# Kernel tuning notes

Measured on AMD Instinct MI355X. Metric: run time of the kernel, lower is better.

The kernel has to match this reference:

```python
import jax, jax.numpy as jnp
import numpy as np

S, B, D = 2048, 1, 4096
H, HKV, DH = 32, 8, 128
THETA = 10000.0


def _rope_tables(seq_len, dim, theta):
    inv_freq = 1.0 / (theta ** (jnp.arange(0, dim, 2, dtype=jnp.float32) / dim))
    freqs = jnp.arange(seq_len, dtype=jnp.float32)[:, None] * inv_freq[None, :]  # [S, DH/2]
    return jnp.cos(freqs), jnp.sin(freqs)


def _apply_rope(x, cos, sin):
    # x: [B, H, S, DH]; non-interleaved (flash_attn interleaved=False) rotation
    half = x.shape[-1] // 2
    x1, x2 = x[..., :half], x[..., half:]
    c = cos[None, None, :, :]
    s = sin[None, None, :, :]
    return jnp.concatenate([x1 * c - x2 * s, x2 * c + x1 * s], axis=-1)


def setup_inputs() -> dict:
    key = jax.random.key(0)
    k1, k2, k3 = jax.random.split(key, 3)
    hidden_states = jax.random.normal(k1, (S, B, D), dtype=jnp.float32)
    W_qkv = jax.random.normal(k2, (D, (H + 2 * HKV) * DH), dtype=jnp.float32) * 0.02
    W_o = jax.random.normal(k3, (H * DH, D), dtype=jnp.float32) * 0.02
    sequence_mask = jnp.ones((B, S), dtype=jnp.int32)
    return {"hidden_states": hidden_states, "sequence_mask": sequence_mask,
            "W_qkv": W_qkv, "W_o": W_o}


def reference(hidden_states, sequence_mask, W_qkv, W_o):
    s, b, _ = hidden_states.shape
    qkv = hidden_states @ W_qkv  # [S, B, (H+2*HKV)*DH]
    q, k, v = jnp.split(qkv, [H * DH, H * DH + HKV * DH], axis=-1)
    q = q.reshape(s, b, H, DH).transpose(1, 2, 0, 3)    # [B, H, S, DH]
    k = k.reshape(s, b, HKV, DH).transpose(1, 2, 0, 3)  # [B, HKV, S, DH]
    v = v.reshape(s, b, HKV, DH).transpose(1, 2, 0, 3)

    cos, sin = _rope_tables(s, DH, THETA)
    q = _apply_rope(q, cos, sin)
    k = _apply_rope(k, cos, sin)

    # GQA: repeat kv heads
    rep = H // HKV
    k = jnp.repeat(k, rep, axis=1)  # [B, H, S, DH]
    v = jnp.repeat(v, rep, axis=1)

    scale = 1.0 / jnp.sqrt(jnp.asarray(DH, dtype=q.dtype))
    scores = jnp.einsum('bhqd,bhkd->bhqk', q, k) * scale
    causal = jnp.tril(jnp.ones((s, s), dtype=bool))
    scores = jnp.where(causal[None, None, :, :], scores, jnp.finfo(scores.dtype).min)
    attn = jax.nn.softmax(scores, axis=-1)
    ctx = jnp.einsum('bhqk,bhkd->bhqd', attn, v)  # [B, H, S, DH]
    ctx = ctx.transpose(2, 0, 1, 3).reshape(s, b, H * DH)  # [S, B, H*DH]
    out = ctx @ W_o  # [S, B, D]
    return out
```

## Files before the change

### kernel.cpp

```cpp
#include <hip/hip_runtime.h>

typedef unsigned short u16;
typedef __bf16 bf16x8 __attribute__((ext_vector_type(8)));
typedef float f32x4 __attribute__((ext_vector_type(4)));
typedef u16 u16x4 __attribute__((ext_vector_type(4)));

constexpr int SEQ = 2048;
constexpr int NQKV = 6144;

__device__ __forceinline__ float bf2f(u16 x) {
    unsigned int u = ((unsigned int)x) << 16;
    return __builtin_bit_cast(float, u);
}
__device__ __forceinline__ u16 f2bf(float f) {
    unsigned int u = __builtin_bit_cast(unsigned int, f);
    u += 0x7FFF + ((u >> 16) & 1);
    return (u16)(u >> 16);
}

__device__ __forceinline__ void gload16(const void* g, void* l) {
    void* gg = const_cast<void*>(g);
    __builtin_amdgcn_global_load_lds(
        (__attribute__((address_space(1))) void*)gg,
        (__attribute__((address_space(3))) void*)l, 16, 0, 0);
}

__device__ __forceinline__ void gatebar(int G) {
    if (G == 8) asm volatile("s_waitcnt vmcnt(8)" ::: "memory");
    else if (G == 4) asm volatile("s_waitcnt vmcnt(4)" ::: "memory");
    else if (G == 3) asm volatile("s_waitcnt vmcnt(3)" ::: "memory");
    else if (G == 2) asm volatile("s_waitcnt vmcnt(2)" ::: "memory");
    else asm volatile("s_waitcnt vmcnt(0)" ::: "memory");
    __builtin_amdgcn_sched_barrier(0);
    __builtin_amdgcn_s_barrier();
    __builtin_amdgcn_sched_barrier(0);
}

__global__ void rope_table_k(float* __restrict__ tab) {
    int idx = blockIdx.x * 256 + threadIdx.x;
    if (idx >= SEQ * 64) return;
    int s = idx >> 6;
    int i = idx & 63;
    float invf = expf(-(float)i * (float)(1.0 / 64.0) * logf(10000.0f));
    float ang = (float)s * invf;
    float sv, cv;
    sincosf(ang, &sv, &cv);
    tab[idx * 2] = cv;
    tab[idx * 2 + 1] = sv;
}

__global__ __launch_bounds__(256) void cast_k(const float* __restrict__ src,
                                              u16* __restrict__ dst, int n4) {
    int i = blockIdx.x * 256 + threadIdx.x;
    if (i >= n4) return;
    f32x4 v = *(const f32x4*)&src[(size_t)i * 4];
    u16x4 o;
#pragma unroll
    for (int j = 0; j < 4; ++j) o[j] = f2bf(v[j]);
    *(u16x4*)&dst[(size_t)i * 4] = o;
}

__global__ __launch_bounds__(256) void transpose_cast_k(const float* __restrict__ src,
                                                        u16* __restrict__ dst, int R, int C) {
    __shared__ u16 tile[64][65];
    int t = threadIdx.x;
    int bx = blockIdx.x, by = blockIdx.y;
    int r0 = by * 64, c0 = bx * 64;
#pragma unroll
    for (int it = 0; it < 4; ++it) {
        int row = it * 16 + (t >> 4);
        int col = (t & 15) * 4;
        f32x4 v = *(const f32x4*)&src[(size_t)(r0 + row) * C + c0 + col];
        tile[row][col] = f2bf(v[0]); tile[row][col + 1] = f2bf(v[1]);
        tile[row][col + 2] = f2bf(v[2]); tile[row][col + 3] = f2bf(v[3]);
    }
    __syncthreads();
#pragma unroll
    for (int it = 0; it < 4; ++it) {
        int orow = it * 16 + (t >> 4);
        int ocol = (t & 15) * 4;
        u16x4 v;
        v[0] = tile[ocol][orow]; v[1] = tile[ocol + 1][orow];
        v[2] = tile[ocol + 2][orow]; v[3] = tile[ocol + 3][orow];
        *(u16x4*)&dst[(size_t)(c0 + orow) * R + r0 + ocol] = v;
    }
}

__global__ __launch_bounds__(256) void transpose_vt_k(const u16* __restrict__ QKV,
                                                      u16* __restrict__ VTg) {
    __shared__ u16 tile[64][65];
    int t = threadIdx.x;
    int s0 = blockIdx.x * 64;
    int hv = blockIdx.y >> 1;
    int d0 = (blockIdx.y & 1) * 64;
    const u16* src = QKV + (size_t)s0 * NQKV + 5120 + hv * 128 + d0;
#pragma unroll
    for (int it = 0; it < 4; ++it) {
        int row = it * 16 + (t >> 4);
        int col = (t & 15) * 4;
        u16x4 v = *(const u16x4*)&src[(size_t)row * NQKV + col];
        tile[row][col] = v[0]; tile[row][col + 1] = v[1];
        tile[row][col + 2] = v[2]; tile[row][col + 3] = v[3];
    }
    __syncthreads();
    u16* dst = VTg + (size_t)hv * 128 * SEQ + (size_t)d0 * SEQ + s0;
#pragma unroll
    for (int it = 0; it < 4; ++it) {
        int orow = it * 16 + (t >> 4);
        int ocol = (t & 15) * 4;
        u16x4 v;
        v[0] = tile[ocol][orow]; v[1] = tile[ocol + 1][orow];
        v[2] = tile[ocol + 2][orow]; v[3] = tile[ocol + 3][orow];
        *(u16x4*)&dst[(size_t)orow * SEQ + ocol] = v;
    }
}

__global__ __launch_bounds__(512, 2) void gemm1_big_k(const u16* __restrict__ A,
                                                      const u16* __restrict__ BT,
                                                      u16* __restrict__ C) {
    constexpr int K = 4096, N = 6144;
    constexpr int SBUF = 57344;
    __shared__ alignas(16) char lds[2 * SBUF];

    int t = threadIdx.x;
    int lane = t & 63, w = t >> 6;
    int wr = w >> 2, wc = w & 3;
    int l15 = lane & 15, l4 = lane >> 4;

    int wg = blockIdx.x;
    int xcd = wg & 7, j = wg >> 3;
    int bm = ((xcd >> 2) << 2) + (j >> 3);
    int bn = ((xcd & 3) << 3) + (j & 7);

    const u16* Ab = A + (size_t)bm * 256 * K;
    const u16* Bb = BT + (size_t)bn * 192 * K;

    const u16* ga[4]; int da[4];
#pragma unroll
    for (int i = 0; i < 4; ++i) {
        int c = t + i * 512;
        int row = c >> 3;
        int ch = (c & 7) ^ (row & 7);
        ga[i] = Ab + (size_t)row * K + ch * 8;
        da[i] = c * 16;
    }
    const u16* gb[3]; int db[3];
#pragma unroll
    for (int i = 0; i < 3; ++i) {
        int c = t + i * 512;
        int row = c >> 3;
        int ch = (c & 7) ^ (row & 7);
        gb[i] = Bb + (size_t)row * K + ch * 8;
        db[i] = 32768 + c * 16;
    }

    auto stage = [&](int kt) {
        char* L = lds + (kt & 1) * SBUF;
        int ko = kt * 64;
#pragma unroll
        for (int i = 0; i < 4; ++i) gload16(ga[i] + ko, L + da[i]);
#pragma unroll
        for (int i = 0; i < 3; ++i) gload16(gb[i] + ko, L + db[i]);
    };

    f32x4 acc[8][3];
#pragma unroll
    for (int i = 0; i < 8; ++i)
#pragma unroll
        for (int j2 = 0; j2 < 3; ++j2) acc[i][j2] = f32x4{0.f, 0.f, 0.f, 0.f};

    int arow[8];
#pragma unroll
    for (int fm = 0; fm < 8; ++fm) arow[fm] = wr * 128 + fm * 16 + l15;
    int brow[3];
#pragma unroll
    for (int fn = 0; fn < 3; ++fn) brow[fn] = wc * 48 + fn * 16 + l15;

    stage(0);
    gatebar(0);

    for (int kt = 0; kt < 64; ++kt) {
        const u16* L = (const u16*)(lds + (kt & 1) * SBUF);
        if (kt + 1 < 64) stage(kt + 1);
        bf16x8 bf[3][2];
#pragma unroll
        for (int fn = 0; fn < 3; ++fn)
#pragma unroll
            for (int kk = 0; kk < 2; ++kk) {
                int ch = (kk * 4 + l4) ^ (brow[fn] & 7);
                bf[fn][kk] = *(const bf16x8*)&L[16384 + brow[fn] * 64 + ch * 8];
            }
#pragma unroll
        for (int p = 0; p < 4; ++p) {
            bf16x8 af[2][2];
#pragma unroll
            for (int f2 = 0; f2 < 2; ++f2)
#pragma unroll
                for (int kk = 0; kk < 2; ++kk) {
                    int r = arow[p * 2 + f2];
                    int ch = (kk * 4 + l4) ^ (r & 7);
                    af[f2][kk] = *(const bf16x8*)&L[r * 64 + ch * 8];
                }
            __builtin_amdgcn_s_setprio(1);
#pragma unroll
            for (int f2 = 0; f2 < 2; ++f2)
#pragma unroll
                for (int kk = 0; kk < 2; ++kk)
#pragma unroll
                    for (int fn = 0; fn < 3; ++fn)
                        acc[p * 2 + f2][fn] = __builtin_amdgcn_mfma_f32_16x16x32_bf16(
                            af[f2][kk], bf[fn][kk], acc[p * 2 + f2][fn], 0, 0, 0);
            __builtin_amdgcn_s_setprio(0);
        }
        gatebar(0);
    }

#pragma unroll
    for (int fm = 0; fm < 8; ++fm)
#pragma unroll
        for (int fn = 0; fn < 3; ++fn)
#pragma unroll
            for (int i = 0; i < 4; ++i) {
                int row = bm * 256 + wr * 128 + fm * 16 + l4 * 4 + i;
                int col = bn * 192 + wc * 48 + fn * 16 + l15;
                C[(size_t)row * N + col] = f2bf(acc[fm][fn][i]);
            }
}

__global__ __launch_bounds__(512, 2) void gemm2_big_k(const u16* __restrict__ A,
                                                      const u16* __restrict__ BT,
                                                      float* __restrict__ C) {
    constexpr int K = 4096, N = 4096;
    constexpr int SBUF = 49152;
    __shared__ alignas(16) char lds[2 * SBUF];

    int t = threadIdx.x;
    int lane = t & 63, w = t >> 6;
    int wr = w >> 2, wc = w & 3;
    int l15 = lane & 15, l4 = lane >> 4;

    int wg = blockIdx.x;
    int xcd = wg & 7, j = wg >> 3;
    int bm = ((xcd >> 2) << 2) + (j >> 3);
    int bn = ((xcd & 3) << 3) + (j & 7);

    const u16* Ab = A + (size_t)bm * 256 * K;
    const u16* Bb = BT + (size_t)bn * 128 * K;

    const u16* ga[4]; int da[4];
#pragma unroll
    for (int i = 0; i < 4; ++i) {
        int c = t + i * 512;
        int row = c >> 3;
        int ch = (c & 7) ^ (row & 7);
        ga[i] = Ab + (size_t)row * K + ch * 8;
        da[i] = c * 16;
    }
    const u16* gb[2]; int db[2];
#pragma unroll
    for (int i = 0; i < 2; ++i) {
        int c = t + i * 512;
        int row = c >> 3;
        int ch = (c & 7) ^ (row & 7);
        gb[i] = Bb + (size_t)row * K + ch * 8;
        db[i] = 32768 + c * 16;
    }

    auto stage = [&](int kt) {
        char* L = lds + (kt & 1) * SBUF;
        int ko = kt * 64;
#pragma unroll
        for (int i = 0; i < 4; ++i) gload16(ga[i] + ko, L + da[i]);
#pragma unroll
        for (int i = 0; i < 2; ++i) gload16(gb[i] + ko, L + db[i]);
    };

    f32x4 acc[8][2];
#pragma unroll
    for (int i = 0; i < 8; ++i)
#pragma unroll
        for (int j2 = 0; j2 < 2; ++j2) acc[i][j2] = f32x4{0.f, 0.f, 0.f, 0.f};

    int arow[8];
#pragma unroll
    for (int fm = 0; fm < 8; ++fm) arow[fm] = wr * 128 + fm * 16 + l15;
    int brow[2];
#pragma unroll
    for (int fn = 0; fn < 2; ++fn) brow[fn] = wc * 32 + fn * 16 + l15;

    stage(0);
    gatebar(0);

    for (int kt = 0; kt < 64; ++kt) {
        const u16* L = (const u16*)(lds + (kt & 1) * SBUF);
        if (kt + 1 < 64) stage(kt + 1);
        bf16x8 bf[2][2];
#pragma unroll
        for (int fn = 0; fn < 2; ++fn)
#pragma unroll
            for (int kk = 0; kk < 2; ++kk) {
                int ch = (kk * 4 + l4) ^ (brow[fn] & 7);
                bf[fn][kk] = *(const bf16x8*)&L[16384 + brow[fn] * 64 + ch * 8];
            }
#pragma unroll
        for (int p = 0; p < 4; ++p) {
            bf16x8 af[2][2];
#pragma unroll
            for (int f2 = 0; f2 < 2; ++f2)
#pragma unroll
                for (int kk = 0; kk < 2; ++kk) {
                    int r = arow[p * 2 + f2];
                    int ch = (kk * 4 + l4) ^ (r & 7);
                    af[f2][kk] = *(const bf16x8*)&L[r * 64 + ch * 8];
                }
            __builtin_amdgcn_s_setprio(1);
#pragma unroll
            for (int f2 = 0; f2 < 2; ++f2)
#pragma unroll
                for (int kk = 0; kk < 2; ++kk)
#pragma unroll
                    for (int fn = 0; fn < 2; ++fn)
                        acc[p * 2 + f2][fn] = __builtin_amdgcn_mfma_f32_16x16x32_bf16(
                            af[f2][kk], bf[fn][kk], acc[p * 2 + f2][fn], 0, 0, 0);
            __builtin_amdgcn_s_setprio(0);
        }
        gatebar(0);
    }

#pragma unroll
    for (int fm = 0; fm < 8; ++fm)
#pragma unroll
        for (int fn = 0; fn < 2; ++fn)
#pragma unroll
            for (int i = 0; i < 4; ++i) {
                int row = bm * 256 + wr * 128 + fm * 16 + l4 * 4 + i;
                int col = bn * 128 + wc * 32 + fn * 16 + l15;
                C[(size_t)row * N + col] = acc[fm][fn][i];
            }
}

__global__ __launch_bounds__(256) void repack_rope_k(const u16* __restrict__ QKV,
                                                     const float* __restrict__ tab,
                                                     u16* __restrict__ Qo, u16* __restrict__ Ko) {
    int idx = blockIdx.x * 256 + threadIdx.x;
    int i4 = (idx & 15) * 4;
    int su = idx >> 4;
    int u = su % 40;
    int s = su / 40;
    const float* tp = tab + (s * 64 + i4) * 2;
    f32x4 t0 = *(const f32x4*)tp;
    f32x4 t1 = *(const f32x4*)(tp + 4);
    float cv[4] = {t0[0], t0[2], t1[0], t1[2]};
    float sv[4] = {t0[1], t0[3], t1[1], t1[3]};
    const u16* base;
    u16* ob;
    if (u < 32) {
        base = QKV + (size_t)s * NQKV + u * 128;
        ob = Qo + ((size_t)u * SEQ + s) * 128;
    } else {
        base = QKV + (size_t)s * NQKV + 4096 + (u - 32) * 128;
        ob = Ko + ((size_t)(u - 32) * SEQ + s) * 128;
    }
    u16x4 x1 = *(const u16x4*)(base + i4);
    u16x4 x2 = *(const u16x4*)(base + 64 + i4);
    u16x4 o1, o2;
#pragma unroll
    for (int j = 0; j < 4; ++j) {
        float a = bf2f(x1[j]), b = bf2f(x2[j]);
        o1[j] = f2bf(a * cv[j] - b * sv[j]);
        o2[j] = f2bf(b * cv[j] + a * sv[j]);
    }
    *(u16x4*)(ob + i4) = o1;
    *(u16x4*)(ob + 64 + i4) = o2;
}

__global__ __launch_bounds__(512) void attn_k(const u16* __restrict__ Qg,
                                              const u16* __restrict__ Kg,
                                              const u16* __restrict__ VTg,
                                              u16* __restrict__ ctx) {
    constexpr float SCL2 = 0.08838834764831845f * 1.44269504088896340736f;
    constexpr float THR = 11.5f;
    __shared__ alignas(16) u16 Klds[2][128 * 128];
    __shared__ alignas(16) u16 VTl[2][128 * 128];
    __shared__ alignas(16) u16 Plds[8 * 16 * 72];

    int t = threadIdx.x;
    int lane = t & 63, w = t >> 6;
    int l15 = lane & 15, l4 = lane >> 4;
    int bx = blockIdx.x;
    int h = blockIdx.y, hkv = h >> 2;
    const u16* Kh = Kg + (size_t)hkv * SEQ * 128;
    const u16* Vh = VTg + (size_t)hkv * 128 * SEQ;
    u16* Pw = &Plds[w * 1152];

    int kr[4], kchs[4];
#pragma unroll
    for (int i2 = 0; i2 < 4; ++i2) {
        int c = t + i2 * 512;
        kr[i2] = c >> 4;
        kchs[i2] = (c & 15) ^ (kr[i2] & 7);
    }
    int vd[4], vchs[4];
#pragma unroll
    for (int i2 = 0; i2 < 4; ++i2) {
        int c = t + i2 * 512;
        vd[i2] = c >> 4;
        vchs[i2] = (c & 15) ^ (vd[i2] & 7);
    }

    int q0 = bx * 128;
    int ntA = bx + 1;

    bf16x8 qf[4];
    f32x4 o[8];
    float m_i[4], l_i[4];

    auto kvbase = [&](int tt) { return (tt < ntA ? tt : tt - ntA) << 7; };
    auto load_q = [&]() {
        const u16* Qh = Qg + ((size_t)h * SEQ + q0 + w * 16 + l15) * 128;
#pragma unroll
        for (int ks = 0; ks < 4; ++ks) qf[ks] = *(const bf16x8*)(Qh + ks * 32 + l4 * 8);
    };
    auto reset_acc = [&]() {
#pragma unroll
        for (int nf = 0; nf < 8; ++nf) o[nf] = f32x4{0.f, 0.f, 0.f, 0.f};
#pragma unroll
        for (int i = 0; i < 4; ++i) { m_i[i] = -3.0e38f; l_i[i] = 0.f; }
    };
    auto write_ctx = [&]() {
        float inv[4];
#pragma unroll
        for (int i = 0; i < 4; ++i) {
            float rs = l_i[i];
            rs += __shfl_xor(rs, 1);
            rs += __shfl_xor(rs, 2);
            rs += __shfl_xor(rs, 4);
            rs += __shfl_xor(rs, 8);
            inv[i] = 1.0f / rs;
        }
#pragma unroll
        for (int nf = 0; nf < 8; ++nf)
#pragma unroll
            for (int i = 0; i < 4; ++i) {
                int qrow = q0 + w * 16 + l4 * 4 + i;
                ctx[(size_t)qrow * 4096 + h * 128 + nf * 16 + l15] = f2bf(o[nf][i] * inv[i]);
            }
    };
    auto stage = [&](int tt) {
        int kv0 = kvbase(tt);
        const u16* Kt = Kh + (size_t)kv0 * 128;
        char* kb = (char*)Klds[tt & 1];
        char* vb = (char*)VTl[tt & 1];
#pragma unroll
        for (int i2 = 0; i2 < 4; ++i2)
            gload16(Kt + kr[i2] * 128 + kchs[i2] * 8, kb + (size_t)(t + i2 * 512) * 16);
#pragma unroll
        for (int i2 = 0; i2 < 4; ++i2)
            gload16(Vh + (size_t)vd[i2] * SEQ + kv0 + vchs[i2] * 8,
                    vb + (size_t)(t + i2 * 512) * 16);
    };

    load_q();
    reset_acc();
    stage(0);

    for (int tt = 0; tt < 17; ++tt) {
        __builtin_amdgcn_s_barrier();
        __builtin_amdgcn_sched_barrier(0);
        bool nxt = (tt + 1 < 17);
        if (nxt) stage(tt + 1);
        gatebar(nxt ? 8 : 0);
        if (tt == ntA) {
            write_ctx();
            q0 = (15 - bx) * 128;
            load_q();
            reset_acc();
        }

        int b = tt & 1;
        int kv0 = kvbase(tt);
        const u16* KL = Klds[b];
        const u16* VL = VTl[b];

        f32x4 sa[8];
#pragma unroll
        for (int cg = 0; cg < 8; ++cg) {
            sa[cg] = f32x4{0.f, 0.f, 0.f, 0.f};
            int row = cg * 16 + l15;
#pragma unroll
            for (int ks = 0; ks < 4; ++ks) {
                int chs = (ks * 4 + l4) ^ (row & 7);
                bf16x8 kf = *(const bf16x8*)&KL[row * 128 + chs * 8];
                sa[cg] = __builtin_amdgcn_mfma_f32_16x16x32_bf16(qf[ks], kf, sa[cg], 0, 0, 0);
            }
        }
#pragma unroll
        for (int cg = 0; cg < 8; ++cg)
#pragma unroll
            for (int i = 0; i < 4; ++i) sa[cg][i] *= SCL2;
        if (kv0 + 127 > q0 + w * 16) {
#pragma unroll
            for (int cg = 0; cg < 8; ++cg) {
                int col = kv0 + cg * 16 + l15;
#pragma unroll
                for (int i = 0; i < 4; ++i) {
                    int qrow = q0 + w * 16 + l4 * 4 + i;
                    if (col > qrow) sa[cg][i] = -3.0e38f;
                }
            }
        }
        float lmx[4];
#pragma unroll
        for (int i = 0; i < 4; ++i) {
            float a0 = fmaxf(fmaxf(sa[0][i], sa[1][i]), fmaxf(sa[2][i], sa[3][i]));
            float a1 = fmaxf(fmaxf(sa[4][i], sa[5][i]), fmaxf(sa[6][i], sa[7][i]));
            lmx[i] = fmaxf(a0, a1);
        }
        bool defer = __all((lmx[0] <= m_i[0] + THR) & (lmx[1] <= m_i[1] + THR) &
                           (lmx[2] <= m_i[2] + THR) & (lmx[3] <= m_i[3] + THR));
        if (!defer) {
            float corr[4];
#pragma unroll
            for (int i = 0; i < 4; ++i) {
                float m0 = lmx[i];
                m0 = fmaxf(m0, __shfl_xor(m0, 1));
                m0 = fmaxf(m0, __shfl_xor(m0, 2));
                m0 = fmaxf(m0, __shfl_xor(m0, 4));
                m0 = fmaxf(m0, __shfl_xor(m0, 8));
                float mnew = fmaxf(m_i[i], m0);
                corr[i] = __builtin_amdgcn_exp2f(m_i[i] - mnew);
                m_i[i] = mnew;
                l_i[i] *= corr[i];
            }
#pragma unroll
            for (int nf = 0; nf < 8; ++nf) {
                o[nf][0] *= corr[0]; o[nf][1] *= corr[1];
                o[nf][2] *= corr[2]; o[nf][3] *= corr[3];
            }
        }
#pragma unroll
        for (int hf = 0; hf < 2; ++hf) {
#pragma unroll
            for (int i = 0; i < 4; ++i) {
                int prow = l4 * 4 + i;
                int sw = (prow >> 1) & 3;
                float rs = 0.f;
#pragma unroll
                for (int cg = 0; cg < 4; ++cg) {
                    float p = __builtin_amdgcn_exp2f(sa[hf * 4 + cg][i] - m_i[i]);
                    rs += p;
                    int ch = cg * 2 + (l15 >> 3);
                    Pw[prow * 72 + ((ch ^ sw) << 3) + (l15 & 7)] = f2bf(p);
                }
                l_i[i] += rs;
            }
            asm volatile("s_waitcnt lgkmcnt(0)" ::: "memory");
            __builtin_amdgcn_sched_barrier(0);
#pragma unroll
            for (int kst = 0; kst < 2; ++kst) {
                int pchs = (kst * 4 + l4) ^ ((l15 >> 1) & 3);
                bf16x8 pf = *(const bf16x8*)&Pw[l15 * 72 + pchs * 8];
                int kst2 = hf * 2 + kst;
#pragma unroll
                for (int nf = 0; nf < 8; ++nf) {
                    int d = nf * 16 + l15;
                    int vch = (kst2 * 4 + l4) ^ (d & 7);
                    bf16x8 vf = *(const bf16x8*)&VL[d * 128 + vch * 8];
                    o[nf] = __builtin_amdgcn_mfma_f32_16x16x32_bf16(pf, vf, o[nf], 0, 0, 0);
                }
            }
        }
    }
    write_ctx();
}

extern "C" void kernel_launch(void* const* d_in, const int* in_sizes, int n_in,
                              void* d_out, int out_size, void* d_ws, size_t ws_size,
                              hipStream_t stream) {
    const float* hidden = (const float*)d_in[0];
    const float* Wqkv = (const float*)d_in[2];
    const float* Wo = (const float*)d_in[3];
    float* out = (float*)d_out;
    char* ws = (char*)d_ws;

    u16* WqkvT   = (u16*)(ws + 0);
    u16* Qb      = (u16*)(ws + 0);
    u16* Kb      = (u16*)(ws + 16777216);
    u16* VTg     = (u16*)(ws + 20971520);
    u16* WoT     = (u16*)(ws + 25165824);
    u16* QKV     = (u16*)(ws + 50331648);
    u16* ctx     = (u16*)(ws + 58720256);
    float* tab   = (float*)(ws + 75497472);
    u16* hiddenB = (u16*)(ws + 76546048);

    rope_table_k<<<512, 256, 0, stream>>>(tab);
    cast_k<<<8192, 256, 0, stream>>>(hidden, hiddenB, 2048 * 4096 / 4);
    transpose_cast_k<<<dim3(96, 64), 256, 0, stream>>>(Wqkv, WqkvT, 4096, 6144);
    gemm1_big_k<<<256, 512, 0, stream>>>(hiddenB, WqkvT, QKV);
    repack_rope_k<<<5120, 256, 0, stream>>>(QKV, tab, Qb, Kb);
    transpose_vt_k<<<dim3(32, 16), 256, 0, stream>>>(QKV, VTg);
    transpose_cast_k<<<dim3(64, 64), 256, 0, stream>>>(Wo, WoT, 4096, 4096);
    attn_k<<<dim3(8, 32), 512, 0, stream>>>(Qb, Kb, VTg, ctx);
    gemm2_big_k<<<256, 512, 0, stream>>>(ctx, WoT, out);
}
```

Baseline: 306.2 us.

## Load GEMM B-operand fragments directly from global into registers, bypassing LDS

In both projection GEMMs the B tile is no longer staged through shared memory. Each wave now loads its own B fragments straight from global memory into double-buffered registers one k-step ahead, and the barrier waits only on the A loads. This shrinks the LDS footprint and removes the B LDS writes and reads. In exchange, B global reads are duplicated across the two wave rows, register pressure rises, and per-lane 16-byte global reads may coalesce less well.

```diff
diff --git a/kernel.cpp b/kernel.cpp
--- a/kernel.cpp
+++ b/kernel.cpp
@@ -27,6 +27,7 @@
 
 __device__ __forceinline__ void gatebar(int G) {
     if (G == 8) asm volatile("s_waitcnt vmcnt(8)" ::: "memory");
+    else if (G == 6) asm volatile("s_waitcnt vmcnt(6)" ::: "memory");
     else if (G == 4) asm volatile("s_waitcnt vmcnt(4)" ::: "memory");
     else if (G == 3) asm volatile("s_waitcnt vmcnt(3)" ::: "memory");
     else if (G == 2) asm volatile("s_waitcnt vmcnt(2)" ::: "memory");
@@ -119,7 +120,7 @@
                                                       const u16* __restrict__ BT,
                                                       u16* __restrict__ C) {
     constexpr int K = 4096, N = 6144;
-    constexpr int SBUF = 57344;
+    constexpr int SBUF = 32768;
     __shared__ alignas(16) char lds[2 * SBUF];
 
     int t = threadIdx.x;
@@ -144,23 +145,29 @@
         ga[i] = Ab + (size_t)row * K + ch * 8;
         da[i] = c * 16;
     }
-    const u16* gb[3]; int db[3];
-#pragma unroll
-    for (int i = 0; i < 3; ++i) {
-        int c = t + i * 512;
-        int row = c >> 3;
-        int ch = (c & 7) ^ (row & 7);
-        gb[i] = Bb + (size_t)row * K + ch * 8;
-        db[i] = 32768 + c * 16;
-    }
-
-    auto stage = [&](int kt) {
+    auto stageA = [&](int kt) {
         char* L = lds + (kt & 1) * SBUF;
         int ko = kt * 64;
 #pragma unroll
         for (int i = 0; i < 4; ++i) gload16(ga[i] + ko, L + da[i]);
-#pragma unroll
-        for (int i = 0; i < 3; ++i) gload16(gb[i] + ko, L + db[i]);
+    };
+
+    int brow[3];
+#pragma unroll
+    for (int fn = 0; fn < 3; ++fn) brow[fn] = wc * 48 + fn * 16 + l15;
+    const u16* gB[3][2];
+#pragma unroll
+    for (int fn = 0; fn < 3; ++fn)
+#pragma unroll
+        for (int kk = 0; kk < 2; ++kk)
+            gB[fn][kk] = Bb + (size_t)brow[fn] * K + (kk * 4 + l4) * 8;
+    auto loadB = [&](bf16x8 (&bf)[3][2], int kt) {
+        int ko = kt * 64;
+#pragma unroll
+        for (int fn = 0; fn < 3; ++fn)
+#pragma unroll
+            for (int kk = 0; kk < 2; ++kk)
+                bf[fn][kk] = *(const bf16x8*)(gB[fn][kk] + ko);
     };
 
     f32x4 acc[8][3];
@@ -172,24 +179,19 @@
     int arow[8];
 #pragma unroll
     for (int fm = 0; fm < 8; ++fm) arow[fm] = wr * 128 + fm * 16 + l15;
-    int brow[3];
-#pragma unroll
-    for (int fn = 0; fn < 3; ++fn) brow[fn] = wc * 48 + fn * 16 + l15;
-
-    stage(0);
+
+    bf16x8 bf0[3][2], bf1[3][2];
+    stageA(0);
+    loadB(bf0, 0);
     gatebar(0);
 
-    for (int kt = 0; kt < 64; ++kt) {
+    auto body = [&](bf16x8 (&bfC)[3][2], bf16x8 (&bfN)[3][2], int kt) {
         const u16* L = (const u16*)(lds + (kt & 1) * SBUF);
-        if (kt + 1 < 64) stage(kt + 1);
-        bf16x8 bf[3][2];
-#pragma unroll
-        for (int fn = 0; fn < 3; ++fn)
-#pragma unroll
-            for (int kk = 0; kk < 2; ++kk) {
-                int ch = (kk * 4 + l4) ^ (brow[fn] & 7);
-                bf[fn][kk] = *(const bf16x8*)&L[16384 + brow[fn] * 64 + ch * 8];
-            }
+        bool nxt = kt + 1 < 64;
+        if (nxt) {
+            stageA(kt + 1);
+            loadB(bfN, kt + 1);
+        }
 #pragma unroll
         for (int p = 0; p < 4; ++p) {
             bf16x8 af[2][2];
@@ -209,10 +211,15 @@
 #pragma unroll
                     for (int fn = 0; fn < 3; ++fn)
                         acc[p * 2 + f2][fn] = __builtin_amdgcn_mfma_f32_16x16x32_bf16(
-                            af[f2][kk], bf[fn][kk], acc[p * 2 + f2][fn], 0, 0, 0);
+                            af[f2][kk], bfC[fn][kk], acc[p * 2 + f2][fn], 0, 0, 0);
             __builtin_amdgcn_s_setprio(0);
         }
-        gatebar(0);
+        gatebar(nxt ? 6 : 0);
+    };
+
+    for (int kt = 0; kt < 64; kt += 2) {
+        body(bf0, bf1, kt);
+        body(bf1, bf0, kt + 1);
     }
 
 #pragma unroll
@@ -231,7 +238,7 @@
                                                       const u16* __restrict__ BT,
                                                       float* __restrict__ C) {
     constexpr int K = 4096, N = 4096;
-    constexpr int SBUF = 49152;
+    constexpr int SBUF = 32768;
     __shared__ alignas(16) char lds[2 * SBUF];
 
     int t = threadIdx.x;
@@ -256,23 +263,29 @@
         ga[i] = Ab + (size_t)row * K + ch * 8;
         da[i] = c * 16;
     }
-    const u16* gb[2]; int db[2];
-#pragma unroll
-    for (int i = 0; i < 2; ++i) {
-        int c = t + i * 512;
-        int row = c >> 3;
-        int ch = (c & 7) ^ (row & 7);
-        gb[i] = Bb + (size_t)row * K + ch * 8;
-        db[i] = 32768 + c * 16;
-    }
-
-    auto stage = [&](int kt) {
+    auto stageA = [&](int kt) {
         char* L = lds + (kt & 1) * SBUF;
         int ko = kt * 64;
 #pragma unroll
         for (int i = 0; i < 4; ++i) gload16(ga[i] + ko, L + da[i]);
-#pragma unroll
-        for (int i = 0; i < 2; ++i) gload16(gb[i] + ko, L + db[i]);
+    };
+
+    int brow[2];
+#pragma unroll
+    for (int fn = 0; fn < 2; ++fn) brow[fn] = wc * 32 + fn * 16 + l15;
+    const u16* gB[2][2];
+#pragma unroll
+    for (int fn = 0; fn < 2; ++fn)
+#pragma unroll
+        for (int kk = 0; kk < 2; ++kk)
+            gB[fn][kk] = Bb + (size_t)brow[fn] * K + (kk * 4 + l4) * 8;
+    auto loadB = [&](bf16x8 (&bf)[2][2], int kt) {
+        int ko = kt * 64;
+#pragma unroll
+        for (int fn = 0; fn < 2; ++fn)
+#pragma unroll
+            for (int kk = 0; kk < 2; ++kk)
+                bf[fn][kk] = *(const bf16x8*)(gB[fn][kk] + ko);
     };
 
     f32x4 acc[8][2];
@@ -284,24 +297,19 @@
     int arow[8];
 #pragma unroll
     for (int fm = 0; fm < 8; ++fm) arow[fm] = wr * 128 + fm * 16 + l15;
-    int brow[2];
-#pragma unroll
-    for (int fn = 0; fn < 2; ++fn) brow[fn] = wc * 32 + fn * 16 + l15;
-
-    stage(0);
+
+    bf16x8 bf0[2][2], bf1[2][2];
+    stageA(0);
+    loadB(bf0, 0);
     gatebar(0);
 
-    for (int kt = 0; kt < 64; ++kt) {
+    auto body = [&](bf16x8 (&bfC)[2][2], bf16x8 (&bfN)[2][2], int kt) {
         const u16* L = (const u16*)(lds + (kt & 1) * SBUF);
-        if (kt + 1 < 64) stage(kt + 1);
-        bf16x8 bf[2][2];
-#pragma unroll
-        for (int fn = 0; fn < 2; ++fn)
-#pragma unroll
-            for (int kk = 0; kk < 2; ++kk) {
-                int ch = (kk * 4 + l4) ^ (brow[fn] & 7);
-                bf[fn][kk] = *(const bf16x8*)&L[16384 + brow[fn] * 64 + ch * 8];
-            }
+        bool nxt = kt + 1 < 64;
+        if (nxt) {
+            stageA(kt + 1);
+            loadB(bfN, kt + 1);
+        }
 #pragma unroll
         for (int p = 0; p < 4; ++p) {
             bf16x8 af[2][2];
@@ -321,10 +329,15 @@
 #pragma unroll
                     for (int fn = 0; fn < 2; ++fn)
                         acc[p * 2 + f2][fn] = __builtin_amdgcn_mfma_f32_16x16x32_bf16(
-                            af[f2][kk], bf[fn][kk], acc[p * 2 + f2][fn], 0, 0, 0);
+                            af[f2][kk], bfC[fn][kk], acc[p * 2 + f2][fn], 0, 0, 0);
             __builtin_amdgcn_s_setprio(0);
         }
-        gatebar(0);
+        gatebar(nxt ? 4 : 0);
+    };
+
+    for (int kt = 0; kt < 64; kt += 2) {
+        body(bf0, bf1, kt);
+        body(bf1, bf0, kt + 1);
     }
 
 #pragma unroll
```

New measurement: 389.3 us. 1.27x slower.

## Give each attention wave two 16-row query groups with half the threads

Applied to the files above, without the earlier changes.

The attention kernel now runs 4 waves of 256 threads instead of 8, and each wave handles 32 query rows as two 16-row groups. Each K and V fragment read from LDS is reused for two MFMAs, which halves LDS read traffic per unit of math. The cost is twice the accumulator and score registers per thread, which may lower occupancy or cause spills. Each thread also issues twice as many async loads, so the wait threshold is raised to match.

```diff
diff --git a/kernel.cpp b/kernel.cpp
--- a/kernel.cpp
+++ b/kernel.cpp
@@ -26,9 +26,10 @@
 }
 
 __device__ __forceinline__ void gatebar(int G) {
-    if (G == 8) asm volatile("s_waitcnt vmcnt(8)" ::: "memory");
+    if (G == 16) asm volatile("s_waitcnt vmcnt(16)" ::: "memory");
+    else if (G == 8) asm volatile("s_waitcnt vmcnt(8)" ::: "memory");
+    else if (G == 6) asm volatile("s_waitcnt vmcnt(6)" ::: "memory");
     else if (G == 4) asm volatile("s_waitcnt vmcnt(4)" ::: "memory");
-    else if (G == 3) asm volatile("s_waitcnt vmcnt(3)" ::: "memory");
     else if (G == 2) asm volatile("s_waitcnt vmcnt(2)" ::: "memory");
     else asm volatile("s_waitcnt vmcnt(0)" ::: "memory");
     __builtin_amdgcn_sched_barrier(0);
@@ -374,7 +375,7 @@
     *(u16x4*)(ob + 64 + i4) = o2;
 }
 
-__global__ __launch_bounds__(512) void attn_k(const u16* __restrict__ Qg,
+__global__ __launch_bounds__(256) void attn_k(const u16* __restrict__ Qg,
                                               const u16* __restrict__ Kg,
                                               const u16* __restrict__ VTg,
                                               u16* __restrict__ ctx) {
@@ -382,7 +383,7 @@
     constexpr float THR = 11.5f;
     __shared__ alignas(16) u16 Klds[2][128 * 128];
     __shared__ alignas(16) u16 VTl[2][128 * 128];
-    __shared__ alignas(16) u16 Plds[8 * 16 * 72];
+    __shared__ alignas(16) u16 Plds[4][2][16 * 72];
 
     int t = threadIdx.x;
     int lane = t & 63, w = t >> 6;
@@ -391,19 +392,14 @@
     int h = blockIdx.y, hkv = h >> 2;
     const u16* Kh = Kg + (size_t)hkv * SEQ * 128;
     const u16* Vh = VTg + (size_t)hkv * 128 * SEQ;
-    u16* Pw = &Plds[w * 1152];
-
-    int kr[4], kchs[4];
-#pragma unroll
-    for (int i2 = 0; i2 < 4; ++i2) {
-        int c = t + i2 * 512;
+    u16* Pw[2] = {&Plds[w][0][0], &Plds[w][1][0]};
+
+    int kr[8], kchs[8], vd[8], vchs[8];
+#pragma unroll
+    for (int i2 = 0; i2 < 8; ++i2) {
+        int c = t + i2 * 256;
         kr[i2] = c >> 4;
         kchs[i2] = (c & 15) ^ (kr[i2] & 7);
-    }
-    int vd[4], vchs[4];
-#pragma unroll
-    for (int i2 = 0; i2 < 4; ++i2) {
-        int c = t + i2 * 512;
         vd[i2] = c >> 4;
         vchs[i2] = (c & 15) ^ (vd[i2] & 7);
     }
@@ -411,40 +407,51 @@
     int q0 = bx * 128;
     int ntA = bx + 1;
 
-    bf16x8 qf[4];
-    f32x4 o[8];
-    float m_i[4], l_i[4];
+    bf16x8 qf[2][4];
+    f32x4 o[2][8];
+    float m_i[2][4], l_i[2][4];
 
     auto kvbase = [&](int tt) { return (tt < ntA ? tt : tt - ntA) << 7; };
     auto load_q = [&]() {
-        const u16* Qh = Qg + ((size_t)h * SEQ + q0 + w * 16 + l15) * 128;
-#pragma unroll
-        for (int ks = 0; ks < 4; ++ks) qf[ks] = *(const bf16x8*)(Qh + ks * 32 + l4 * 8);
+#pragma unroll
+        for (int qg = 0; qg < 2; ++qg) {
+            const u16* Qh = Qg + ((size_t)h * SEQ + q0 + w * 32 + qg * 16 + l15) * 128;
+#pragma unroll
+            for (int ks = 0; ks < 4; ++ks)
+                qf[qg][ks] = *(const bf16x8*)(Qh + ks * 32 + l4 * 8);
+        }
     };
     auto reset_acc = [&]() {
 #pragma unroll
-        for (int nf = 0; nf < 8; ++nf) o[nf] = f32x4{0.f, 0.f, 0.f, 0.f};
-#pragma unroll
-        for (int i = 0; i < 4; ++i) { m_i[i] = -3.0e38f; l_i[i] = 0.f; }
+        for (int qg = 0; qg < 2; ++qg) {
+#pragma unroll
+            for (int nf = 0; nf < 8; ++nf) o[qg][nf] = f32x4{0.f, 0.f, 0.f, 0.f};
+#pragma unroll
+            for (int i = 0; i < 4; ++i) { m_i[qg][i] = -3.0e38f; l_i[qg][i] = 0.f; }
+        }
     };
     auto write_ctx = [&]() {
-        float inv[4];
-#pragma unroll
-        for (int i = 0; i < 4; ++i) {
-            float rs = l_i[i];
-            rs += __shfl_xor(rs, 1);
-            rs += __shfl_xor(rs, 2);
-            rs += __shfl_xor(rs, 4);
-            rs += __shfl_xor(rs, 8);
-            inv[i] = 1.0f / rs;
-        }
-#pragma unroll
-        for (int nf = 0; nf < 8; ++nf)
+#pragma unroll
+        for (int qg = 0; qg < 2; ++qg) {
+            float inv[4];
 #pragma unroll
             for (int i = 0; i < 4; ++i) {
-                int qrow = q0 + w * 16 + l4 * 4 + i;
-                ctx[(size_t)qrow * 4096 + h * 128 + nf * 16 + l15] = f2bf(o[nf][i] * inv[i]);
-            }
+                float rs = l_i[qg][i];
+                rs += __shfl_xor(rs, 1);
+                rs += __shfl_xor(rs, 2);
+                rs += __shfl_xor(rs, 4);
+                rs += __shfl_xor(rs, 8);
+                inv[i] = 1.0f / rs;
+            }
+#pragma unroll
+            for (int nf = 0; nf < 8; ++nf)
+#pragma unroll
+                for (int i = 0; i < 4; ++i) {
+                    int qrow = q0 + w * 32 + qg * 16 + l4 * 4 + i;
+                    ctx[(size_t)qrow * 4096 + h * 128 + nf * 16 + l15] =
+                        f2bf(o[qg][nf][i] * inv[i]);
+                }
+        }
     };
     auto stage = [&](int tt) {
         int kv0 = kvbase(tt);
@@ -452,12 +459,12 @@
         char* kb = (char*)Klds[tt & 1];
         char* vb = (char*)VTl[tt & 1];
 #pragma unroll
-        for (int i2 = 0; i2 < 4; ++i2)
-            gload16(Kt + kr[i2] * 128 + kchs[i2] * 8, kb + (size_t)(t + i2 * 512) * 16);
-#pragma unroll
-        for (int i2 = 0; i2 < 4; ++i2)
+        for (int i2 = 0; i2 < 8; ++i2)
+            gload16(Kt + kr[i2] * 128 + kchs[i2] * 8, kb + (size_t)(t + i2 * 256) * 16);
+#pragma unroll
+        for (int i2 = 0; i2 < 8; ++i2)
             gload16(Vh + (size_t)vd[i2] * SEQ + kv0 + vchs[i2] * 8,
-                    vb + (size_t)(t + i2 * 512) * 16);
+                    vb + (size_t)(t + i2 * 256) * 16);
     };
 
     load_q();
@@ -469,7 +476,7 @@
         __builtin_amdgcn_sched_barrier(0);
         bool nxt = (tt + 1 < 17);
         if (nxt) stage(tt + 1);
-        gatebar(nxt ? 8 : 0);
+        gatebar(nxt ? 16 : 0);
         if (tt == ntA) {
             write_ctx();
             q0 = (15 - bx) * 128;
@@ -482,91 +489,115 @@
         const u16* KL = Klds[b];
         const u16* VL = VTl[b];
 
-        f32x4 sa[8];
+        f32x4 sa[2][8];
+#pragma unroll
+        for (int qg = 0; qg < 2; ++qg)
+#pragma unroll
+            for (int cg = 0; cg < 8; ++cg) sa[qg][cg] = f32x4{0.f, 0.f, 0.f, 0.f};
 #pragma unroll
         for (int cg = 0; cg < 8; ++cg) {
-            sa[cg] = f32x4{0.f, 0.f, 0.f, 0.f};
             int row = cg * 16 + l15;
 #pragma unroll
             for (int ks = 0; ks < 4; ++ks) {
                 int chs = (ks * 4 + l4) ^ (row & 7);
                 bf16x8 kf = *(const bf16x8*)&KL[row * 128 + chs * 8];
-                sa[cg] = __builtin_amdgcn_mfma_f32_16x16x32_bf16(qf[ks], kf, sa[cg], 0, 0, 0);
-            }
-        }
-#pragma unroll
-        for (int cg = 0; cg < 8; ++cg)
-#pragma unroll
-            for (int i = 0; i < 4; ++i) sa[cg][i] *= SCL2;
-        if (kv0 + 127 > q0 + w * 16) {
-#pragma unroll
-            for (int cg = 0; cg < 8; ++cg) {
-                int col = kv0 + cg * 16 + l15;
+                sa[0][cg] = __builtin_amdgcn_mfma_f32_16x16x32_bf16(qf[0][ks], kf,
+                                                                   sa[0][cg], 0, 0, 0);
+                sa[1][cg] = __builtin_amdgcn_mfma_f32_16x16x32_bf16(qf[1][ks], kf,
+                                                                   sa[1][cg], 0, 0, 0);
+            }
+        }
+#pragma unroll
+        for (int qg = 0; qg < 2; ++qg)
+#pragma unroll
+            for (int cg = 0; cg < 8; ++cg)
+#pragma unroll
+                for (int i = 0; i < 4; ++i) sa[qg][cg][i] *= SCL2;
+        if (kv0 + 127 > q0 + w * 32) {
+#pragma unroll
+            for (int qg = 0; qg < 2; ++qg)
+#pragma unroll
+                for (int cg = 0; cg < 8; ++cg) {
+                    int col = kv0 + cg * 16 + l15;
+#pragma unroll
+                    for (int i = 0; i < 4; ++i) {
+                        int qrow = q0 + w * 32 + qg * 16 + l4 * 4 + i;
+                        if (col > qrow) sa[qg][cg][i] = -3.0e38f;
+                    }
+                }
+        }
+        float lmx[2][4];
+#pragma unroll
+        for (int qg = 0; qg < 2; ++qg)
+#pragma unroll
+            for (int i = 0; i < 4; ++i) {
+                float a0 = fmaxf(fmaxf(sa[qg][0][i], sa[qg][1][i]),
+                                 fmaxf(sa[qg][2][i], sa[qg][3][i]));
+                float a1 = fmaxf(fmaxf(sa[qg][4][i], sa[qg][5][i]),
+                                 fmaxf(sa[qg][6][i], sa[qg][7][i]));
+                lmx[qg][i] = fmaxf(a0, a1);
+            }
+        bool defer = __all(
+            (lmx[0][0] <= m_i[0][0] + THR) & (lmx[0][1] <= m_i[0][1] + THR) &
+            (lmx[0][2] <= m_i[0][2] + THR) & (lmx[0][3] <= m_i[0][3] + THR) &
+            (lmx[1][0] <= m_i[1][0] + THR) & (lmx[1][1] <= m_i[1][1] + THR) &
+            (lmx[1][2] <= m_i[1][2] + THR) & (lmx[1][3] <= m_i[1][3] + THR));
+        if (!defer) {
+#pragma unroll
+            for (int qg = 0; qg < 2; ++qg) {
+                float corr[4];
 #pragma unroll
                 for (int i = 0; i < 4; ++i) {
-                    int qrow = q0 + w * 16 + l4 * 4 + i;
-                    if (col > qrow) sa[cg][i] = -3.0e38f;
-                }
-            }
-        }
-        float lmx[4];
-#pragma unroll
-        for (int i = 0; i < 4; ++i) {
-            float a0 = fmaxf(fmaxf(sa[0][i], sa[1][i]), fmaxf(sa[2][i], sa[3][i]));
-            float a1 = fmaxf(fmaxf(sa[4][i], sa[5][i]), fmaxf(sa[6][i], sa[7][i]));
-            lmx[i] = fmaxf(a0, a1);
-        }
-        bool defer = __all((lmx[0] <= m_i[0] + THR) & (lmx[1] <= m_i[1] + THR) &
-                           (lmx[2] <= m_i[2] + THR) & (lmx[3] <= m_i[3] + THR));
-        if (!defer) {
-            float corr[4];
-#pragma unroll
-            for (int i = 0; i < 4; ++i) {
-                float m0 = lmx[i];
-                m0 = fmaxf(m0, __shfl_xor(m0, 1));
-                m0 = fmaxf(m0, __shfl_xor(m0, 2));
-                m0 = fmaxf(m0, __shfl_xor(m0, 4));
-                m0 = fmaxf(m0, __shfl_xor(m0, 8));
-                float mnew = fmaxf(m_i[i], m0);
-                corr[i] = __builtin_amdgcn_exp2f(m_i[i] - mnew);
-                m_i[i] = mnew;
-                l_i[i] *= corr[i];
-            }
-#pragma unroll
-            for (int nf = 0; nf < 8; ++nf) {
-                o[nf][0] *= corr[0]; o[nf][1] *= corr[1];
-                o[nf][2] *= corr[2]; o[nf][3] *= corr[3];
+                    float m0 = lmx[qg][i];
+                    m0 = fmaxf(m0, __shfl_xor(m0, 1));
+                    m0 = fmaxf(m0, __shfl_xor(m0, 2));
+                    m0 = fmaxf(m0, __shfl_xor(m0, 4));
+                    m0 = fmaxf(m0, __shfl_xor(m0, 8));
+                    float mnew = fmaxf(m_i[qg][i], m0);
+                    corr[i] = __builtin_amdgcn_exp2f(m_i[qg][i] - mnew);
+                    m_i[qg][i] = mnew;
+                    l_i[qg][i] *= corr[i];
+                }
+#pragma unroll
+                for (int nf = 0; nf < 8; ++nf) {
+                    o[qg][nf][0] *= corr[0]; o[qg][nf][1] *= corr[1];
+                    o[qg][nf][2] *= corr[2]; o[qg][nf][3] *= corr[3];
+                }
             }
         }
 #pragma unroll
         for (int hf = 0; hf < 2; ++hf) {
 #pragma unroll
-            for (int i = 0; i < 4; ++i) {
-                int prow = l4 * 4 + i;
-                int sw = (prow >> 1) & 3;
-                float rs = 0.f;
-#pragma unroll
-                for (int cg = 0; cg < 4; ++cg) {
-                    float p = __builtin_amdgcn_exp2f(sa[hf * 4 + cg][i] - m_i[i]);
-                    rs += p;
-                    int ch = cg * 2 + (l15 >> 3);
-                    Pw[prow * 72 + ((ch ^ sw) << 3) + (l15 & 7)] = f2bf(p);
-                }
-                l_i[i] += rs;
-            }
+            for (int qg = 0; qg < 2; ++qg)
+#pragma unroll
+                for (int i = 0; i < 4; ++i) {
+                    int prow = l4 * 4 + i;
+                    int sw = (prow >> 1) & 3;
+                    float rs = 0.f;
+#pragma unroll
+                    for (int cg = 0; cg < 4; ++cg) {
+                        float p = __builtin_amdgcn_exp2f(sa[qg][hf * 4 + cg][i] - m_i[qg][i]);
+                        rs += p;
+                        int ch = cg * 2 + (l15 >> 3);
+                        Pw[qg][prow * 72 + ((ch ^ sw) << 3) + (l15 & 7)] = f2bf(p);
+                    }
+                    l_i[qg][i] += rs;
+                }
             asm volatile("s_waitcnt lgkmcnt(0)" ::: "memory");
             __builtin_amdgcn_sched_barrier(0);
 #pragma unroll
             for (int kst = 0; kst < 2; ++kst) {
                 int pchs = (kst * 4 + l4) ^ ((l15 >> 1) & 3);
-                bf16x8 pf = *(const bf16x8*)&Pw[l15 * 72 + pchs * 8];
+                bf16x8 pf0 = *(const bf16x8*)&Pw[0][l15 * 72 + pchs * 8];
+                bf16x8 pf1 = *(const bf16x8*)&Pw[1][l15 * 72 + pchs * 8];
                 int kst2 = hf * 2 + kst;
 #pragma unroll
                 for (int nf = 0; nf < 8; ++nf) {
                     int d = nf * 16 + l15;
                     int vch = (kst2 * 4 + l4) ^ (d & 7);
                     bf16x8 vf = *(const bf16x8*)&VL[d * 128 + vch * 8];
-                    o[nf] = __builtin_amdgcn_mfma_f32_16x16x32_bf16(pf, vf, o[nf], 0, 0, 0);
+                    o[0][nf] = __builtin_amdgcn_mfma_f32_16x16x32_bf16(pf0, vf, o[0][nf], 0, 0, 0);
+                    o[1][nf] = __builtin_amdgcn_mfma_f32_16x16x32_bf16(pf1, vf, o[1][nf], 0, 0, 0);
                 }
             }
         }
@@ -600,6 +631,6 @@
     repack_rope_k<<<5120, 256, 0, stream>>>(QKV, tab, Qb, Kb);
     transpose_vt_k<<<dim3(32, 16), 256, 0, stream>>>(QKV, VTg);
     transpose_cast_k<<<dim3(64, 64), 256, 0, stream>>>(Wo, WoT, 4096, 4096);
-    attn_k<<<dim3(8, 32), 512, 0, stream>>>(Qb, Kb, VTg, ctx);
+    attn_k<<<dim3(8, 32), 256, 0, stream>>>(Qb, Kb, VTg, ctx);
     gemm2_big_k<<<256, 512, 0, stream>>>(ctx, WoT, out);
 }
```

Result: slower. 317.7 us (+3.8%).
